# Kernel optimization log

Measured on AMD Instinct MI355X. Metric: run time of the kernel, lower is better.

The kernel has to match this reference:

```python
import jax, jax.numpy as jnp
import numpy as np

PI2 = 2.0 * np.pi
ZITTER = 1e-4
TEMP = 0.1          # tempering0
LIKERR_BOUND = (0.1, 1.0)
GUMBEL_EPS = 1e-20


def setup_inputs() -> dict:
    key = jax.random.key(0)
    ks = jax.random.split(key, 12)
    nb, nd, ndim, nch = 8, 768, 1, 3
    nmix, h, ns = 5, 10, 10
    def xavier(k, shape):
        fan_in, fan_out = shape[1], shape[0]
        lim = np.sqrt(6.0 / (fan_in + fan_out))
        return jax.random.uniform(k, shape, jnp.float32, -lim, lim)
    return {
        "xc": jax.random.normal(ks[0], (nb, nd, ndim, nch), jnp.float32),
        "yc": jax.random.normal(ks[1], (nb, nd, nch), jnp.float32),
        "mu": jax.random.uniform(ks[2], (nmix, ndim), jnp.float32),
        "inv_std": jax.random.uniform(ks[3], (nmix, ndim), jnp.float32),
        "likerr": jax.random.uniform(ks[4], (nch,), jnp.float32),
        "unif": jax.random.uniform(ks[5], (nb, ns, nch, nmix), jnp.float32),
        "W1": xavier(ks[6], (h, nmix + 1)), "b1": jnp.zeros((h,), jnp.float32),
        "W2": xavier(ks[7], (h, h * nch)), "b2": jnp.zeros((h,), jnp.float32),
        "W3": xavier(ks[8], (h, h)), "b3": jnp.zeros((h,), jnp.float32),
        "W4": xavier(ks[9], (h, h)), "b4": jnp.zeros((h,), jnp.float32),
        "W5": xavier(ks[10], (nmix * nch, h)), "b5": jnp.zeros((nmix * nch,), jnp.float32),
    }


def _sm_kernel_mix(xc, mu, inv_std):
    """Spectral-mixture kernel per mixture: (nb,nmix,nd,nd,nch)."""
    exp_x = xc[:, None] * inv_std[None, :, None, :, None]   # (nb,nmix,nd,ndim,nch)
    cos_x = xc[:, None] * mu[None, :, None, :, None]
    e2 = jnp.sum(exp_x ** 2, axis=-2)                        # (nb,nmix,nd,nch)
    cross = jnp.einsum('bmadk,bmcdk->bmack', exp_x, exp_x)   # (nb,nmix,nd,nd,nch)
    exp_term = e2[:, :, :, None, :] + e2[:, :, None, :, :] - 2.0 * cross
    c1 = jnp.sum(cos_x, axis=-2)                             # (nb,nmix,nd,nch)
    cos_term = c1[:, :, :, None, :] - c1[:, :, None, :, :]
    return jnp.exp(-0.5 * PI2 ** 2 * exp_term) * jnp.cos(PI2 * cos_term)


def reference(xc, yc, mu, inv_std, likerr, unif,
              W1, b1, W2, b2, W3, b3, W4, b4, W5, b5):
    nb, nd, ndim, nch = xc.shape
    nmix = mu.shape[0]
    outs = _sm_kernel_mix(xc, mu, inv_std)                   # (nb,nmix,nd,nd,nch)

    # --- trans-invariant weight net (logits=None kernel path + zitter eye) ---
    # feature[b,i,c,m] = sum_j (K + zitter*I)[b,m,i,j,c] * yc[b,j,c]
    feature = jnp.einsum('bmijc,bjc->bicm', outs, yc) + ZITTER * yc[:, :, :, None]
    tif = jnp.concatenate([feature, yc[..., None]], axis=-1) # (nb,nd,nch,nmix+1)
    hh = jax.nn.relu(tif @ W1.T + b1)                        # (nb,nd,nch,h)
    hh = hh.mean(axis=1).reshape(nb, -1)                     # (nb,nch*h)
    hh = jax.nn.relu(hh @ W2.T + b2)
    hh = jax.nn.relu(hh @ W3.T + b3)
    hh = jax.nn.relu(hh @ W4.T + b4)
    loglogits = (hh @ W5.T + b5).reshape(nb, nch, nmix)      # (nb,nch,nmix)

    # --- Gumbel-softmax mixture sampling ---
    g = -jnp.log(-jnp.log(unif + GUMBEL_EPS))                # (nb,ns,nch,nmix)
    y = jax.nn.softmax((g + loglogits[:, None]) / TEMP, axis=-1)
    logits_s = y.mean(axis=1)                                # (nb,nch,nmix)

    # --- weighted mixture reduction + noise diagonal ---
    w = jnp.transpose(logits_s, (0, 2, 1))[:, :, None, None, :]  # (nb,nmix,1,1,nch)
    weighted = jnp.sum(outs * w, axis=1)                     # (nb,nd,nd,nch)
    likerr_c = jnp.clip(likerr, LIKERR_BOUND[0], LIKERR_BOUND[1])
    eye = jnp.eye(nd, dtype=xc.dtype)
    weighted = weighted + (ZITTER + likerr_c ** 2)[None, None, None, :] * eye[None, :, :, None]
    return weighted
```

## Files before the change

### kernel.cpp

```cpp
#include <hip/hip_runtime.h>
#include <hip/hip_bf16.h>

#define NB 8
#define ND 768
#define NCH 3
#define NMIX 5
#define NH 10
#define NS 10

#define HALF_PI2SQ 19.739208802178716f
#define EXP2_SCALE 28.47780760903922f
#define ZITTERF 1e-4f

__device__ __forceinline__ void sincos2pi(float t, float& s, float& c) {
    const float f = __builtin_amdgcn_fractf(t);
    s = __builtin_amdgcn_sinf(f);
    c = __builtin_amdgcn_cosf(f);
}

__global__ void __launch_bounds__(256) feature_kernel(
        const float* __restrict__ xc, const float* __restrict__ yc,
        const float* __restrict__ mu, const float* __restrict__ istd,
        float* __restrict__ tif) {
    const int wid  = (blockIdx.x << 2) + (threadIdx.x >> 6);
    const int lane = threadIdx.x & 63;
    const int b   = wid / (NCH * (ND / 4));
    const int rem = wid % (NCH * (ND / 4));
    const int c   = rem / (ND / 4);
    const int i0  = (rem % (ND / 4)) * 4;

    float cmu[NMIX], ce2[NMIX];
#pragma unroll
    for (int m = 0; m < NMIX; ++m) {
        const float is = istd[m];
        cmu[m] = mu[m];
        ce2[m] = -EXP2_SCALE * is * is;
    }

    float xi[4], ci[4][NMIX], si[4][NMIX];
#pragma unroll
    for (int t = 0; t < 4; ++t) {
        xi[t] = xc[(b * ND + i0 + t) * NCH + c];
#pragma unroll
        for (int m = 0; m < NMIX; ++m)
            sincos2pi(cmu[m] * xi[t], si[t][m], ci[t][m]);
    }

    float acc[4][NMIX];
#pragma unroll
    for (int t = 0; t < 4; ++t)
#pragma unroll
        for (int m = 0; m < NMIX; ++m) acc[t][m] = 0.f;

    for (int j = lane; j < ND; j += 64) {
        const float xj = xc[(b * ND + j) * NCH + c];
        const float yj = yc[(b * ND + j) * NCH + c];
        float cj[NMIX], sj[NMIX];
#pragma unroll
        for (int m = 0; m < NMIX; ++m)
            sincos2pi(cmu[m] * xj, sj[m], cj[m]);
#pragma unroll
        for (int t = 0; t < 4; ++t) {
            const float dx  = xi[t] - xj;
            const float dx2 = dx * dx;
#pragma unroll
            for (int m = 0; m < NMIX; ++m) {
                const float e  = __builtin_amdgcn_exp2f(ce2[m] * dx2);
                const float cv = fmaf(ci[t][m], cj[m], si[t][m] * sj[m]);
                acc[t][m] = fmaf(e * cv, yj, acc[t][m]);
            }
        }
    }

#pragma unroll
    for (int t = 0; t < 4; ++t)
#pragma unroll
        for (int m = 0; m < NMIX; ++m)
            for (int off = 32; off; off >>= 1)
                acc[t][m] += __shfl_down(acc[t][m], off);

    if (lane == 0) {
#pragma unroll
        for (int t = 0; t < 4; ++t) {
            const float yi = yc[(b * ND + i0 + t) * NCH + c];
            float* tp = tif + ((b * ND + i0 + t) * NCH + c) * (NMIX + 1);
#pragma unroll
            for (int m = 0; m < NMIX; ++m) tp[m] = acc[t][m] + ZITTERF * yi;
            tp[NMIX] = yi;
        }
    }
}

__global__ void __launch_bounds__(256) mlp_gumbel_kernel(
        const float* __restrict__ tif,
        const float* __restrict__ W1, const float* __restrict__ b1,
        const float* __restrict__ W2, const float* __restrict__ b2,
        const float* __restrict__ W3, const float* __restrict__ b3,
        const float* __restrict__ W4, const float* __restrict__ b4,
        const float* __restrict__ W5, const float* __restrict__ b5,
        const float* __restrict__ unif,
        float* __restrict__ wout) {
    const int b   = blockIdx.x;
    const int tid = threadIdx.x;

    __shared__ float sW1[NH * 6], sW2[NH * NCH * NH], sW3[NH * NH], sW4[NH * NH],
                     sW5[NCH * NMIX * NH];
    __shared__ float sb1[NH], sb2[NH], sb3[NH], sb4[NH], sb5[NCH * NMIX];
    __shared__ float red[4][NCH * NH];
    __shared__ float hvec[NCH * NH], h2[NH], h3[NH], h4[NH], ll[NCH * NMIX], wacc[NCH * NMIX];

    if (tid < NH * 6) sW1[tid] = W1[tid];
    for (int t = tid; t < NH * NCH * NH; t += 256) sW2[t] = W2[t];
    if (tid < NH * NH) sW3[tid] = W3[tid];
    if (tid < NH * NH) sW4[tid] = W4[tid];
    if (tid < NCH * NMIX * NH) sW5[tid] = W5[tid];
    if (tid < NH) { sb1[tid] = b1[tid]; sb2[tid] = b2[tid]; sb3[tid] = b3[tid]; sb4[tid] = b4[tid]; }
    if (tid < NCH * NMIX) { sb5[tid] = b5[tid]; wacc[tid] = 0.f; }
    __syncthreads();

    float part[NCH * NH];
#pragma unroll
    for (int t = 0; t < NCH * NH; ++t) part[t] = 0.f;

    for (int ii = tid; ii < ND; ii += 256) {
        for (int c = 0; c < NCH; ++c) {
            const float* tp = tif + ((b * ND + ii) * NCH + c) * (NMIX + 1);
            float f[6];
#pragma unroll
            for (int m = 0; m < 6; ++m) f[m] = tp[m];
#pragma unroll
            for (int k = 0; k < NH; ++k) {
                float a = sb1[k];
#pragma unroll
                for (int m = 0; m < 6; ++m) a += f[m] * sW1[k * 6 + m];
                part[c * NH + k] += fmaxf(a, 0.f);
            }
        }
    }

#pragma unroll
    for (int t = 0; t < NCH * NH; ++t)
        for (int off = 32; off; off >>= 1)
            part[t] += __shfl_down(part[t], off);

    const int lane = tid & 63, wv = tid >> 6;
    if (lane == 0)
        for (int t = 0; t < NCH * NH; ++t) red[wv][t] = part[t];
    __syncthreads();

    if (tid < NCH * NH)
        hvec[tid] = (red[0][tid] + red[1][tid] + red[2][tid] + red[3][tid]) * (1.f / (float)ND);
    __syncthreads();

    if (tid < NH) {
        float a = sb2[tid];
#pragma unroll
        for (int j = 0; j < NCH * NH; ++j) a += sW2[tid * (NCH * NH) + j] * hvec[j];
        h2[tid] = fmaxf(a, 0.f);
    }
    __syncthreads();
    if (tid < NH) {
        float a = sb3[tid];
#pragma unroll
        for (int j = 0; j < NH; ++j) a += sW3[tid * NH + j] * h2[j];
        h3[tid] = fmaxf(a, 0.f);
    }
    __syncthreads();
    if (tid < NH) {
        float a = sb4[tid];
#pragma unroll
        for (int j = 0; j < NH; ++j) a += sW4[tid * NH + j] * h3[j];
        h4[tid] = fmaxf(a, 0.f);
    }
    __syncthreads();
    if (tid < NCH * NMIX) {
        float a = sb5[tid];
#pragma unroll
        for (int j = 0; j < NH; ++j) a += sW5[tid * NH + j] * h4[j];
        ll[tid] = a;
    }
    __syncthreads();

    if (tid < NS * NCH) {
        const int s = tid / NCH, c = tid % NCH;
        float z[NMIX], zmax = -1e30f;
#pragma unroll
        for (int m = 0; m < NMIX; ++m) {
            const float u = unif[((b * NS + s) * NCH + c) * NMIX + m];
            const float g = -__logf(-__logf(u + 1e-20f));
            z[m] = (g + ll[c * NMIX + m]) * 10.0f;
            zmax = fmaxf(zmax, z[m]);
        }
        float e[NMIX], se = 0.f;
#pragma unroll
        for (int m = 0; m < NMIX; ++m) { e[m] = __expf(z[m] - zmax); se += e[m]; }
        const float inv = 0.1f / se;
#pragma unroll
        for (int m = 0; m < NMIX; ++m)
            atomicAdd(&wacc[c * NMIX + m], e[m] * inv);
    }
    __syncthreads();
    if (tid < NCH * NMIX) wout[b * (NCH * NMIX) + tid] = wacc[tid];
}

__global__ void __launch_bounds__(256) weighted_kernel(
        const float* __restrict__ xc, const float* __restrict__ wmix,
        const float* __restrict__ mu, const float* __restrict__ istd,
        const float* __restrict__ likerr,
        float* __restrict__ out) {
    const int b   = blockIdx.x / ((ND / 4) * (ND / 256));
    const int rem = blockIdx.x % ((ND / 4) * (ND / 256));
    const int i0  = (rem / (ND / 256)) * 4;
    const int j   = (rem % (ND / 256)) * 256 + threadIdx.x;
    const int tid = threadIdx.x;

    __shared__ float2 strig[4][NCH][NMIX];

    if (tid < 4 * NCH * NMIX) {
        const int it = tid / (NCH * NMIX);
        const int r  = tid % (NCH * NMIX);
        const int cc = r / NMIX, m = r % NMIX;
        const float x = xc[(b * ND + i0 + it) * NCH + cc];
        float s, co;
        sincos2pi(mu[m] * x, s, co);
        strig[it][cc][m] = make_float2(co, s);
    }
    __syncthreads();

    float cmu[NMIX], ce2[NMIX], w[NCH * NMIX], diag[NCH];
#pragma unroll
    for (int m = 0; m < NMIX; ++m) {
        const float is = istd[m];
        cmu[m] = mu[m];
        ce2[m] = -EXP2_SCALE * is * is;
    }
#pragma unroll
    for (int t = 0; t < NCH * NMIX; ++t) w[t] = wmix[b * (NCH * NMIX) + t];
#pragma unroll
    for (int c = 0; c < NCH; ++c) {
        const float lk = fminf(fmaxf(likerr[c], 0.1f), 1.0f);
        diag[c] = ZITTERF + lk * lk;
    }

    float xj[NCH], cj[NCH][NMIX], sj[NCH][NMIX];
#pragma unroll
    for (int c = 0; c < NCH; ++c) {
        xj[c] = xc[(b * ND + j) * NCH + c];
#pragma unroll
        for (int m = 0; m < NMIX; ++m)
            sincos2pi(cmu[m] * xj[c], sj[c][m], cj[c][m]);
    }

#pragma unroll
    for (int it = 0; it < 4; ++it) {
        const int i = i0 + it;
        float res[NCH];
#pragma unroll
        for (int c = 0; c < NCH; ++c) {
            const float xi  = xc[(b * ND + i) * NCH + c];
            const float dx  = xi - xj[c];
            const float dx2 = dx * dx;
            float a = 0.f;
#pragma unroll
            for (int m = 0; m < NMIX; ++m) {
                const float2 t2 = strig[it][c][m];
                const float e   = __builtin_amdgcn_exp2f(ce2[m] * dx2);
                const float cv  = fmaf(t2.x, cj[c][m], t2.y * sj[c][m]);
                a = fmaf(w[c * NMIX + m], e * cv, a);
            }
            if (i == j) a += diag[c];
            res[c] = a;
        }
        float* op = out + (size_t)((b * ND + i) * ND + j) * NCH;
        op[0] = res[0];
        op[1] = res[1];
        op[2] = res[2];
    }
}

extern "C" void kernel_launch(void* const* d_in, const int* in_sizes, int n_in,
                              void* d_out, int out_size, void* d_ws, size_t ws_size,
                              hipStream_t stream) {
    const float* xc     = (const float*)d_in[0];
    const float* yc     = (const float*)d_in[1];
    const float* mu     = (const float*)d_in[2];
    const float* istd   = (const float*)d_in[3];
    const float* likerr = (const float*)d_in[4];
    const float* unif   = (const float*)d_in[5];
    const float* W1 = (const float*)d_in[6];  const float* b1 = (const float*)d_in[7];
    const float* W2 = (const float*)d_in[8];  const float* b2 = (const float*)d_in[9];
    const float* W3 = (const float*)d_in[10]; const float* b3 = (const float*)d_in[11];
    const float* W4 = (const float*)d_in[12]; const float* b4 = (const float*)d_in[13];
    const float* W5 = (const float*)d_in[14]; const float* b5 = (const float*)d_in[15];

    float* out  = (float*)d_out;
    float* tif  = (float*)d_ws;
    float* wmix = tif + NB * ND * NCH * (NMIX + 1);

    feature_kernel<<<(NB * NCH * (ND / 4)) / 4, 256, 0, stream>>>(xc, yc, mu, istd, tif);

    mlp_gumbel_kernel<<<NB, 256, 0, stream>>>(tif, W1, b1, W2, b2, W3, b3, W4, b4,
                                              W5, b5, unif, wmix);

    weighted_kernel<<<NB * (ND / 4) * (ND / 256), 256, 0, stream>>>(xc, wmix, mu, istd,
                                                                    likerr, out);
}
```

Measured before the change: 150.6 us.

## Fuse three kernels into one cooperative persistent kernel with grid syncs

Merges the feature, MLP/Gumbel, and weighted-output kernels into a single cooperative kernel. Phases are separated by grid.sync, and each phase uses grid-stride loops over work units. This is meant to remove two kernel launches and the gaps between them. In exchange it adds grid-wide barriers, an occupancy query on every launch, and a grid capped at 1152 blocks. The MLP phase also runs on only 8 blocks while every other block waits at the barrier.

```diff
diff --git a/kernel.cpp b/kernel.cpp
--- a/kernel.cpp
+++ b/kernel.cpp
@@ -1,5 +1,8 @@
 #include <hip/hip_runtime.h>
+#include <hip/hip_cooperative_groups.h>
 #include <hip/hip_bf16.h>
+
+namespace cg = cooperative_groups;
 
 #define NB 8
 #define ND 768
@@ -7,10 +10,13 @@
 #define NMIX 5
 #define NH 10
 #define NS 10
-
-#define HALF_PI2SQ 19.739208802178716f
+#define NUM_CU 256
+
 #define EXP2_SCALE 28.47780760903922f
 #define ZITTERF 1e-4f
+
+#define A_UNITS (NB * NCH * (ND / 4))
+#define C_UNITS (NB * (ND / 4) * (ND / 256))
 
 __device__ __forceinline__ void sincos2pi(float t, float& s, float& c) {
     const float f = __builtin_amdgcn_fractf(t);
@@ -18,290 +24,294 @@
     c = __builtin_amdgcn_cosf(f);
 }
 
-__global__ void __launch_bounds__(256) feature_kernel(
-        const float* __restrict__ xc, const float* __restrict__ yc,
-        const float* __restrict__ mu, const float* __restrict__ istd,
-        float* __restrict__ tif) {
-    const int wid  = (blockIdx.x << 2) + (threadIdx.x >> 6);
-    const int lane = threadIdx.x & 63;
-    const int b   = wid / (NCH * (ND / 4));
-    const int rem = wid % (NCH * (ND / 4));
-    const int c   = rem / (ND / 4);
-    const int i0  = (rem % (ND / 4)) * 4;
+struct Params {
+    const float *xc, *yc, *mu, *istd, *likerr, *unif;
+    const float *W1, *b1, *W2, *b2, *W3, *b3, *W4, *b4, *W5, *b5;
+    float *tif, *wmix, *out;
+};
+
+__global__ void __launch_bounds__(256) fused_kernel(Params p) {
+    cg::grid_group grid = cg::this_grid();
+    const int tid  = threadIdx.x;
+    const int lane = tid & 63;
+
+    __shared__ float sW1[NH * 6], sb1[NH];
+    __shared__ float sW2[NH * NCH * NH], sb2[NH];
+    __shared__ float sW3[NH * NH], sb3[NH];
+    __shared__ float sW4[NH * NH], sb4[NH];
+    __shared__ float sW5[NCH * NMIX * NH], sb5[NCH * NMIX];
+    __shared__ float red[4][NCH * NH];
+    __shared__ float hvec[NCH * NH], h2[NH], h3[NH], h4[NH], ll[NCH * NMIX], wacc[NCH * NMIX];
+    __shared__ float2 strig[4][NCH][NMIX];
 
     float cmu[NMIX], ce2[NMIX];
 #pragma unroll
     for (int m = 0; m < NMIX; ++m) {
-        const float is = istd[m];
-        cmu[m] = mu[m];
+        const float is = p.istd[m];
+        cmu[m] = p.mu[m];
         ce2[m] = -EXP2_SCALE * is * is;
     }
 
-    float xi[4], ci[4][NMIX], si[4][NMIX];
-#pragma unroll
-    for (int t = 0; t < 4; ++t) {
-        xi[t] = xc[(b * ND + i0 + t) * NCH + c];
-#pragma unroll
-        for (int m = 0; m < NMIX; ++m)
-            sincos2pi(cmu[m] * xi[t], si[t][m], ci[t][m]);
+    {
+        const int wid        = blockIdx.x * 4 + (tid >> 6);
+        const int totalWaves = gridDim.x * 4;
+        for (int u = wid; u < A_UNITS; u += totalWaves) {
+            const int b   = u / (NCH * (ND / 4));
+            const int rem = u % (NCH * (ND / 4));
+            const int c   = rem / (ND / 4);
+            const int i0  = (rem % (ND / 4)) * 4;
+
+            float xi[4], ci[4][NMIX], si[4][NMIX];
+#pragma unroll
+            for (int t = 0; t < 4; ++t) {
+                xi[t] = p.xc[(b * ND + i0 + t) * NCH + c];
+#pragma unroll
+                for (int m = 0; m < NMIX; ++m)
+                    sincos2pi(cmu[m] * xi[t], si[t][m], ci[t][m]);
+            }
+
+            float acc[4][NMIX];
+#pragma unroll
+            for (int t = 0; t < 4; ++t)
+#pragma unroll
+                for (int m = 0; m < NMIX; ++m) acc[t][m] = 0.f;
+
+            for (int j = lane; j < ND; j += 64) {
+                const float xj = p.xc[(b * ND + j) * NCH + c];
+                const float yj = p.yc[(b * ND + j) * NCH + c];
+                float cj[NMIX], sj[NMIX];
+#pragma unroll
+                for (int m = 0; m < NMIX; ++m)
+                    sincos2pi(cmu[m] * xj, sj[m], cj[m]);
+#pragma unroll
+                for (int t = 0; t < 4; ++t) {
+                    const float dx  = xi[t] - xj;
+                    const float dx2 = dx * dx;
+#pragma unroll
+                    for (int m = 0; m < NMIX; ++m) {
+                        const float e  = __builtin_amdgcn_exp2f(ce2[m] * dx2);
+                        const float cv = fmaf(ci[t][m], cj[m], si[t][m] * sj[m]);
+                        acc[t][m] = fmaf(e * cv, yj, acc[t][m]);
+                    }
+                }
+            }
+
+#pragma unroll
+            for (int t = 0; t < 4; ++t)
+#pragma unroll
+                for (int m = 0; m < NMIX; ++m)
+                    for (int off = 32; off; off >>= 1)
+                        acc[t][m] += __shfl_down(acc[t][m], off);
+
+            if (lane == 0) {
+#pragma unroll
+                for (int t = 0; t < 4; ++t) {
+                    const float yi = p.yc[(b * ND + i0 + t) * NCH + c];
+                    float* tp = p.tif + ((b * ND + i0 + t) * NCH + c) * (NMIX + 1);
+#pragma unroll
+                    for (int m = 0; m < NMIX; ++m) tp[m] = acc[t][m] + ZITTERF * yi;
+                    tp[NMIX] = yi;
+                }
+            }
+        }
     }
 
-    float acc[4][NMIX];
-#pragma unroll
-    for (int t = 0; t < 4; ++t)
-#pragma unroll
-        for (int m = 0; m < NMIX; ++m) acc[t][m] = 0.f;
-
-    for (int j = lane; j < ND; j += 64) {
-        const float xj = xc[(b * ND + j) * NCH + c];
-        const float yj = yc[(b * ND + j) * NCH + c];
-        float cj[NMIX], sj[NMIX];
-#pragma unroll
-        for (int m = 0; m < NMIX; ++m)
-            sincos2pi(cmu[m] * xj, sj[m], cj[m]);
-#pragma unroll
-        for (int t = 0; t < 4; ++t) {
-            const float dx  = xi[t] - xj;
-            const float dx2 = dx * dx;
+    grid.sync();
+
+    if (blockIdx.x < NB) {
+        const int b = blockIdx.x;
+
+        if (tid < NH * 6) sW1[tid] = p.W1[tid];
+        for (int t = tid; t < NH * NCH * NH; t += 256) sW2[t] = p.W2[t];
+        if (tid < NH * NH) { sW3[tid] = p.W3[tid]; sW4[tid] = p.W4[tid]; }
+        if (tid < NCH * NMIX * NH) sW5[tid] = p.W5[tid];
+        if (tid < NH) { sb1[tid] = p.b1[tid]; sb2[tid] = p.b2[tid];
+                        sb3[tid] = p.b3[tid]; sb4[tid] = p.b4[tid]; }
+        if (tid < NCH * NMIX) { sb5[tid] = p.b5[tid]; wacc[tid] = 0.f; }
+        __syncthreads();
+
+        float part[NCH * NH];
+#pragma unroll
+        for (int t = 0; t < NCH * NH; ++t) part[t] = 0.f;
+
+        for (int ii = tid; ii < ND; ii += 256) {
+            for (int c = 0; c < NCH; ++c) {
+                const float* tp = p.tif + ((b * ND + ii) * NCH + c) * (NMIX + 1);
+                float f[6];
+#pragma unroll
+                for (int m = 0; m < 6; ++m) f[m] = tp[m];
+#pragma unroll
+                for (int k = 0; k < NH; ++k) {
+                    float a = sb1[k];
+#pragma unroll
+                    for (int m = 0; m < 6; ++m) a += f[m] * sW1[k * 6 + m];
+                    part[c * NH + k] += fmaxf(a, 0.f);
+                }
+            }
+        }
+
+#pragma unroll
+        for (int t = 0; t < NCH * NH; ++t)
+            for (int off = 32; off; off >>= 1)
+                part[t] += __shfl_down(part[t], off);
+
+        const int wv = tid >> 6;
+        if (lane == 0)
+            for (int t = 0; t < NCH * NH; ++t) red[wv][t] = part[t];
+        __syncthreads();
+
+        if (tid < NCH * NH)
+            hvec[tid] = (red[0][tid] + red[1][tid] + red[2][tid] + red[3][tid]) * (1.f / (float)ND);
+        __syncthreads();
+
+        if (tid < NH) {
+            float a = sb2[tid];
+#pragma unroll
+            for (int j = 0; j < NCH * NH; ++j) a += sW2[tid * (NCH * NH) + j] * hvec[j];
+            h2[tid] = fmaxf(a, 0.f);
+        }
+        __syncthreads();
+        if (tid < NH) {
+            float a = sb3[tid];
+#pragma unroll
+            for (int j = 0; j < NH; ++j) a += sW3[tid * NH + j] * h2[j];
+            h3[tid] = fmaxf(a, 0.f);
+        }
+        __syncthreads();
+        if (tid < NH) {
+            float a = sb4[tid];
+#pragma unroll
+            for (int j = 0; j < NH; ++j) a += sW4[tid * NH + j] * h3[j];
+            h4[tid] = fmaxf(a, 0.f);
+        }
+        __syncthreads();
+        if (tid < NCH * NMIX) {
+            float a = sb5[tid];
+#pragma unroll
+            for (int j = 0; j < NH; ++j) a += sW5[tid * NH + j] * h4[j];
+            ll[tid] = a;
+        }
+        __syncthreads();
+
+        if (tid < NS * NCH) {
+            const int s = tid / NCH, c = tid % NCH;
+            float z[NMIX], zmax = -1e30f;
 #pragma unroll
             for (int m = 0; m < NMIX; ++m) {
-                const float e  = __builtin_amdgcn_exp2f(ce2[m] * dx2);
-                const float cv = fmaf(ci[t][m], cj[m], si[t][m] * sj[m]);
-                acc[t][m] = fmaf(e * cv, yj, acc[t][m]);
-            }
-        }
+                const float u = p.unif[((b * NS + s) * NCH + c) * NMIX + m];
+                const float g = -__logf(-__logf(u + 1e-20f));
+                z[m] = (g + ll[c * NMIX + m]) * 10.0f;
+                zmax = fmaxf(zmax, z[m]);
+            }
+            float e[NMIX], se = 0.f;
+#pragma unroll
+            for (int m = 0; m < NMIX; ++m) { e[m] = __expf(z[m] - zmax); se += e[m]; }
+            const float inv = 0.1f / se;
+#pragma unroll
+            for (int m = 0; m < NMIX; ++m)
+                atomicAdd(&wacc[c * NMIX + m], e[m] * inv);
+        }
+        __syncthreads();
+        if (tid < NCH * NMIX) p.wmix[b * (NCH * NMIX) + tid] = wacc[tid];
     }
 
-#pragma unroll
-    for (int t = 0; t < 4; ++t)
-#pragma unroll
-        for (int m = 0; m < NMIX; ++m)
-            for (int off = 32; off; off >>= 1)
-                acc[t][m] += __shfl_down(acc[t][m], off);
-
-    if (lane == 0) {
-#pragma unroll
-        for (int t = 0; t < 4; ++t) {
-            const float yi = yc[(b * ND + i0 + t) * NCH + c];
-            float* tp = tif + ((b * ND + i0 + t) * NCH + c) * (NMIX + 1);
-#pragma unroll
-            for (int m = 0; m < NMIX; ++m) tp[m] = acc[t][m] + ZITTERF * yi;
-            tp[NMIX] = yi;
-        }
-    }
-}
-
-__global__ void __launch_bounds__(256) mlp_gumbel_kernel(
-        const float* __restrict__ tif,
-        const float* __restrict__ W1, const float* __restrict__ b1,
-        const float* __restrict__ W2, const float* __restrict__ b2,
-        const float* __restrict__ W3, const float* __restrict__ b3,
-        const float* __restrict__ W4, const float* __restrict__ b4,
-        const float* __restrict__ W5, const float* __restrict__ b5,
-        const float* __restrict__ unif,
-        float* __restrict__ wout) {
-    const int b   = blockIdx.x;
-    const int tid = threadIdx.x;
-
-    __shared__ float sW1[NH * 6], sW2[NH * NCH * NH], sW3[NH * NH], sW4[NH * NH],
-                     sW5[NCH * NMIX * NH];
-    __shared__ float sb1[NH], sb2[NH], sb3[NH], sb4[NH], sb5[NCH * NMIX];
-    __shared__ float red[4][NCH * NH];
-    __shared__ float hvec[NCH * NH], h2[NH], h3[NH], h4[NH], ll[NCH * NMIX], wacc[NCH * NMIX];
-
-    if (tid < NH * 6) sW1[tid] = W1[tid];
-    for (int t = tid; t < NH * NCH * NH; t += 256) sW2[t] = W2[t];
-    if (tid < NH * NH) sW3[tid] = W3[tid];
-    if (tid < NH * NH) sW4[tid] = W4[tid];
-    if (tid < NCH * NMIX * NH) sW5[tid] = W5[tid];
-    if (tid < NH) { sb1[tid] = b1[tid]; sb2[tid] = b2[tid]; sb3[tid] = b3[tid]; sb4[tid] = b4[tid]; }
-    if (tid < NCH * NMIX) { sb5[tid] = b5[tid]; wacc[tid] = 0.f; }
-    __syncthreads();
-
-    float part[NCH * NH];
-#pragma unroll
-    for (int t = 0; t < NCH * NH; ++t) part[t] = 0.f;
-
-    for (int ii = tid; ii < ND; ii += 256) {
+    grid.sync();
+
+    {
+        float diag[NCH];
+#pragma unroll
         for (int c = 0; c < NCH; ++c) {
-            const float* tp = tif + ((b * ND + ii) * NCH + c) * (NMIX + 1);
-            float f[6];
-#pragma unroll
-            for (int m = 0; m < 6; ++m) f[m] = tp[m];
-#pragma unroll
-            for (int k = 0; k < NH; ++k) {
-                float a = sb1[k];
-#pragma unroll
-                for (int m = 0; m < 6; ++m) a += f[m] * sW1[k * 6 + m];
-                part[c * NH + k] += fmaxf(a, 0.f);
-            }
-        }
-    }
-
-#pragma unroll
-    for (int t = 0; t < NCH * NH; ++t)
-        for (int off = 32; off; off >>= 1)
-            part[t] += __shfl_down(part[t], off);
-
-    const int lane = tid & 63, wv = tid >> 6;
-    if (lane == 0)
-        for (int t = 0; t < NCH * NH; ++t) red[wv][t] = part[t];
-    __syncthreads();
-
-    if (tid < NCH * NH)
-        hvec[tid] = (red[0][tid] + red[1][tid] + red[2][tid] + red[3][tid]) * (1.f / (float)ND);
-    __syncthreads();
-
-    if (tid < NH) {
-        float a = sb2[tid];
-#pragma unroll
-        for (int j = 0; j < NCH * NH; ++j) a += sW2[tid * (NCH * NH) + j] * hvec[j];
-        h2[tid] = fmaxf(a, 0.f);
-    }
-    __syncthreads();
-    if (tid < NH) {
-        float a = sb3[tid];
-#pragma unroll
-        for (int j = 0; j < NH; ++j) a += sW3[tid * NH + j] * h2[j];
-        h3[tid] = fmaxf(a, 0.f);
-    }
-    __syncthreads();
-    if (tid < NH) {
-        float a = sb4[tid];
-#pragma unroll
-        for (int j = 0; j < NH; ++j) a += sW4[tid * NH + j] * h3[j];
-        h4[tid] = fmaxf(a, 0.f);
-    }
-    __syncthreads();
-    if (tid < NCH * NMIX) {
-        float a = sb5[tid];
-#pragma unroll
-        for (int j = 0; j < NH; ++j) a += sW5[tid * NH + j] * h4[j];
-        ll[tid] = a;
-    }
-    __syncthreads();
-
-    if (tid < NS * NCH) {
-        const int s = tid / NCH, c = tid % NCH;
-        float z[NMIX], zmax = -1e30f;
-#pragma unroll
-        for (int m = 0; m < NMIX; ++m) {
-            const float u = unif[((b * NS + s) * NCH + c) * NMIX + m];
-            const float g = -__logf(-__logf(u + 1e-20f));
-            z[m] = (g + ll[c * NMIX + m]) * 10.0f;
-            zmax = fmaxf(zmax, z[m]);
-        }
-        float e[NMIX], se = 0.f;
-#pragma unroll
-        for (int m = 0; m < NMIX; ++m) { e[m] = __expf(z[m] - zmax); se += e[m]; }
-        const float inv = 0.1f / se;
-#pragma unroll
-        for (int m = 0; m < NMIX; ++m)
-            atomicAdd(&wacc[c * NMIX + m], e[m] * inv);
-    }
-    __syncthreads();
-    if (tid < NCH * NMIX) wout[b * (NCH * NMIX) + tid] = wacc[tid];
-}
-
-__global__ void __launch_bounds__(256) weighted_kernel(
-        const float* __restrict__ xc, const float* __restrict__ wmix,
-        const float* __restrict__ mu, const float* __restrict__ istd,
-        const float* __restrict__ likerr,
-        float* __restrict__ out) {
-    const int b   = blockIdx.x / ((ND / 4) * (ND / 256));
-    const int rem = blockIdx.x % ((ND / 4) * (ND / 256));
-    const int i0  = (rem / (ND / 256)) * 4;
-    const int j   = (rem % (ND / 256)) * 256 + threadIdx.x;
-    const int tid = threadIdx.x;
-
-    __shared__ float2 strig[4][NCH][NMIX];
-
-    if (tid < 4 * NCH * NMIX) {
-        const int it = tid / (NCH * NMIX);
-        const int r  = tid % (NCH * NMIX);
-        const int cc = r / NMIX, m = r % NMIX;
-        const float x = xc[(b * ND + i0 + it) * NCH + cc];
-        float s, co;
-        sincos2pi(mu[m] * x, s, co);
-        strig[it][cc][m] = make_float2(co, s);
-    }
-    __syncthreads();
-
-    float cmu[NMIX], ce2[NMIX], w[NCH * NMIX], diag[NCH];
-#pragma unroll
-    for (int m = 0; m < NMIX; ++m) {
-        const float is = istd[m];
-        cmu[m] = mu[m];
-        ce2[m] = -EXP2_SCALE * is * is;
-    }
-#pragma unroll
-    for (int t = 0; t < NCH * NMIX; ++t) w[t] = wmix[b * (NCH * NMIX) + t];
-#pragma unroll
-    for (int c = 0; c < NCH; ++c) {
-        const float lk = fminf(fmaxf(likerr[c], 0.1f), 1.0f);
-        diag[c] = ZITTERF + lk * lk;
-    }
-
-    float xj[NCH], cj[NCH][NMIX], sj[NCH][NMIX];
-#pragma unroll
-    for (int c = 0; c < NCH; ++c) {
-        xj[c] = xc[(b * ND + j) * NCH + c];
-#pragma unroll
-        for (int m = 0; m < NMIX; ++m)
-            sincos2pi(cmu[m] * xj[c], sj[c][m], cj[c][m]);
-    }
-
-#pragma unroll
-    for (int it = 0; it < 4; ++it) {
-        const int i = i0 + it;
-        float res[NCH];
-#pragma unroll
-        for (int c = 0; c < NCH; ++c) {
-            const float xi  = xc[(b * ND + i) * NCH + c];
-            const float dx  = xi - xj[c];
-            const float dx2 = dx * dx;
-            float a = 0.f;
-#pragma unroll
-            for (int m = 0; m < NMIX; ++m) {
-                const float2 t2 = strig[it][c][m];
-                const float e   = __builtin_amdgcn_exp2f(ce2[m] * dx2);
-                const float cv  = fmaf(t2.x, cj[c][m], t2.y * sj[c][m]);
-                a = fmaf(w[c * NMIX + m], e * cv, a);
-            }
-            if (i == j) a += diag[c];
-            res[c] = a;
-        }
-        float* op = out + (size_t)((b * ND + i) * ND + j) * NCH;
-        op[0] = res[0];
-        op[1] = res[1];
-        op[2] = res[2];
+            const float lk = fminf(fmaxf(p.likerr[c], 0.1f), 1.0f);
+            diag[c] = ZITTERF + lk * lk;
+        }
+
+        for (int u = blockIdx.x; u < C_UNITS; u += gridDim.x) {
+            const int b   = u / ((ND / 4) * (ND / 256));
+            const int rem = u % ((ND / 4) * (ND / 256));
+            const int i0  = (rem / (ND / 256)) * 4;
+            const int j   = (rem % (ND / 256)) * 256 + tid;
+
+            __syncthreads();
+            if (tid < 4 * NCH * NMIX) {
+                const int it = tid / (NCH * NMIX);
+                const int r  = tid % (NCH * NMIX);
+                const int cc = r / NMIX, m = r % NMIX;
+                const float x = p.xc[(b * ND + i0 + it) * NCH + cc];
+                float s, co;
+                sincos2pi(cmu[m] * x, s, co);
+                strig[it][cc][m] = make_float2(co, s);
+            }
+            __syncthreads();
+
+            float w[NCH * NMIX];
+#pragma unroll
+            for (int t = 0; t < NCH * NMIX; ++t) w[t] = p.wmix[b * (NCH * NMIX) + t];
+
+            float xj[NCH], cj[NCH][NMIX], sj[NCH][NMIX];
+#pragma unroll
+            for (int c = 0; c < NCH; ++c) {
+                xj[c] = p.xc[(b * ND + j) * NCH + c];
+#pragma unroll
+                for (int m = 0; m < NMIX; ++m)
+                    sincos2pi(cmu[m] * xj[c], sj[c][m], cj[c][m]);
+            }
+
+#pragma unroll
+            for (int it = 0; it < 4; ++it) {
+                const int i = i0 + it;
+                float res[NCH];
+#pragma unroll
+                for (int c = 0; c < NCH; ++c) {
+                    const float xi  = p.xc[(b * ND + i) * NCH + c];
+                    const float dx  = xi - xj[c];
+                    const float dx2 = dx * dx;
+                    float a = 0.f;
+#pragma unroll
+                    for (int m = 0; m < NMIX; ++m) {
+                        const float2 t2 = strig[it][c][m];
+                        const float e   = __builtin_amdgcn_exp2f(ce2[m] * dx2);
+                        const float cv  = fmaf(t2.x, cj[c][m], t2.y * sj[c][m]);
+                        a = fmaf(w[c * NMIX + m], e * cv, a);
+                    }
+                    if (i == j) a += diag[c];
+                    res[c] = a;
+                }
+                float* op = p.out + (size_t)((b * ND + i) * ND + j) * NCH;
+                op[0] = res[0];
+                op[1] = res[1];
+                op[2] = res[2];
+            }
+        }
     }
 }
 
 extern "C" void kernel_launch(void* const* d_in, const int* in_sizes, int n_in,
                               void* d_out, int out_size, void* d_ws, size_t ws_size,
                               hipStream_t stream) {
-    const float* xc     = (const float*)d_in[0];
-    const float* yc     = (const float*)d_in[1];
-    const float* mu     = (const float*)d_in[2];
-    const float* istd   = (const float*)d_in[3];
-    const float* likerr = (const float*)d_in[4];
-    const float* unif   = (const float*)d_in[5];
-    const float* W1 = (const float*)d_in[6];  const float* b1 = (const float*)d_in[7];
-    const float* W2 = (const float*)d_in[8];  const float* b2 = (const float*)d_in[9];
-    const float* W3 = (const float*)d_in[10]; const float* b3 = (const float*)d_in[11];
-    const float* W4 = (const float*)d_in[12]; const float* b4 = (const float*)d_in[13];
-    const float* W5 = (const float*)d_in[14]; const float* b5 = (const float*)d_in[15];
-
-    float* out  = (float*)d_out;
     float* tif  = (float*)d_ws;
     float* wmix = tif + NB * ND * NCH * (NMIX + 1);
 
-    feature_kernel<<<(NB * NCH * (ND / 4)) / 4, 256, 0, stream>>>(xc, yc, mu, istd, tif);
-
-    mlp_gumbel_kernel<<<NB, 256, 0, stream>>>(tif, W1, b1, W2, b2, W3, b3, W4, b4,
-                                              W5, b5, unif, wmix);
-
-    weighted_kernel<<<NB * (ND / 4) * (ND / 256), 256, 0, stream>>>(xc, wmix, mu, istd,
-                                                                    likerr, out);
+    Params p;
+    p.xc     = (const float*)d_in[0];
+    p.yc     = (const float*)d_in[1];
+    p.mu     = (const float*)d_in[2];
+    p.istd   = (const float*)d_in[3];
+    p.likerr = (const float*)d_in[4];
+    p.unif   = (const float*)d_in[5];
+    p.W1 = (const float*)d_in[6];  p.b1 = (const float*)d_in[7];
+    p.W2 = (const float*)d_in[8];  p.b2 = (const float*)d_in[9];
+    p.W3 = (const float*)d_in[10]; p.b3 = (const float*)d_in[11];
+    p.W4 = (const float*)d_in[12]; p.b4 = (const float*)d_in[13];
+    p.W5 = (const float*)d_in[14]; p.b5 = (const float*)d_in[15];
+    p.tif = tif; p.wmix = wmix; p.out = (float*)d_out;
+
+    int blocksPerCU = 0;
+    hipOccupancyMaxActiveBlocksPerMultiprocessor(&blocksPerCU, fused_kernel, 256, 0);
+    if (blocksPerCU < 1) blocksPerCU = 1;
+    int grid = blocksPerCU * NUM_CU;
+    if (grid > 1152) grid = 1152;
+
+    void* args[] = { &p };
+    hipLaunchCooperativeKernel((const void*)fused_kernel, dim3(grid), dim3(256),
+                               args, 0, stream);
 }
```

New measurement: 263.8 us. 1.75x slower.
